# Optimization experiments

Measured on AMD Instinct MI355X. Metric: run time of the kernel, lower is better.

## Reference

```python
import jax, jax.numpy as jnp
import numpy as np

K = 1048576          # number of shooting particles (k); x also has K points
LR = 0.25            # fixed-point gradient-descent learning rate
N_ITERS = 20         # nr_of_fixed_point_iterations
nl = jnp.tanh        # nonlinearity='tanh'


def _advect(z, t1, b1, t2, b2):
    # z: [n, 2, 1]; t*: [2,2]; b*: [2,1]. dot z = theta1 @ nl(theta2 @ z + b2) + b1
    return jnp.matmul(t1, nl(jnp.matmul(t2, z) + b2)) + b1


def _lagrangian(t1, b1, t2, b2, q, p, invK, invKb):
    eye = jnp.eye(2, dtype=t1.dtype)
    v1 = t1.reshape(-1)
    v2 = (t2 - eye).reshape(-1)
    kinetic = 0.5 * (v1 @ invK @ v1 + v2 @ invK @ v2
                     + b1[:, 0] @ invKb @ b1[:, 0] + b2[:, 0] @ invKb @ b2[:, 0])
    potential = jnp.mean(p * _advect(q, t1, b1, t2, b2))
    return kinetic - potential


def _run_fixed_point(q, p, t1, b1, t2, b2, invK, invKb):
    grad_fn = jax.grad(_lagrangian, argnums=(0, 1, 2, 3))
    def step(carry, _):
        t1, b1, t2, b2 = carry
        g1, gb1, g2, gb2 = grad_fn(t1, b1, t2, b2, q, p, invK, invKb)
        return (t1 - LR * g1, b1 - LR * gb1, t2 - LR * g2, b2 - LR * gb2), None
    carry, _ = jax.lax.scan(step, (t1, b1, t2, b2), None, length=N_ITERS)
    return carry


def setup_inputs() -> dict:
    key = jax.random.key(0)
    k1, k2, k3, k4, k5 = jax.random.split(key, 5)
    inp = jax.random.normal(k1, (3 * K, 1, 2), dtype=jnp.float32)
    return {
        "t": jnp.zeros((1,), dtype=jnp.float32),
        "inp": inp,
        "theta1_init": jax.random.normal(k2, (2, 2), dtype=jnp.float32),
        "bias1_init": jax.random.normal(k3, (2, 1), dtype=jnp.float32),
        "theta2_init": jax.random.normal(k4, (2, 2), dtype=jnp.float32),
        "bias2_init": jax.random.normal(k5, (2, 1), dtype=jnp.float32),
        "inv_Kbar": jnp.eye(4, dtype=jnp.float32),    # Kbar = I(d^2) -> inverse = I
        "inv_Kbar_b": jnp.eye(2, dtype=jnp.float32),  # Kbar_b = I(d) -> inverse = I
        "k": K,
    }


def reference(t, inp, theta1_init, bias1_init, theta2_init, bias2_init,
              inv_Kbar, inv_Kbar_b, k):
    qt, pt, xt = inp[:k], inp[k:2 * k], inp[2 * k:]
    q = jnp.swapaxes(qt, 1, 2)  # [k, 2, 1]
    p = jnp.swapaxes(pt, 1, 2)
    x = jnp.swapaxes(xt, 1, 2)

    def final_thetas(qv):
        return _run_fixed_point(qv, p, theta1_init, bias1_init,
                                theta2_init, bias2_init, inv_Kbar, inv_Kbar_b)

    t1, b1, t2, b2 = final_thetas(q)

    # dot_p = dL/dq of the final Lagrangian, including dependence of the
    # fixed-point thetas on q (torch uses create_graph=True throughout).
    def L_of_q(qv):
        ft1, fb1, ft2, fb2 = final_thetas(qv)
        return _lagrangian(ft1, fb1, ft2, fb2, qv, p, inv_Kbar, inv_Kbar_b)

    dot_p = jax.grad(L_of_q)(q)
    dot_x = _advect(x, t1, b1, t2, b2)
    dot_q = _advect(q, t1, b1, t2, b2)

    return jnp.concatenate([jnp.swapaxes(dot_q, 1, 2),
                            jnp.swapaxes(dot_p, 1, 2),
                            jnp.swapaxes(dot_x, 1, 2)], axis=0)
```

## Files before the change

kernel.cpp:

```cpp
#include <hip/hip_runtime.h>


#define LR 0.25f
#define NIT 20
#define RTPB 512
#define NBR 256

typedef float v2f __attribute__((ext_vector_type(2)));

__device__ __forceinline__ v2f tanh2(v2f x){
    v2f e;
    e.x = __expf(x.x + x.x);
    e.y = __expf(x.y + x.y);
    v2f d = e + 1.0f;
    v2f r;
    r.x = __builtin_amdgcn_rcpf(d.x);
    r.y = __builtin_amdgcn_rcpf(d.y);
    return 1.0f - (r + r);
}

#define DPP_ADD(x, ctrl) ((x) + __int_as_float(__builtin_amdgcn_update_dpp(0, __float_as_int(x), (ctrl), 0xF, 0xF, true)))
__device__ __forceinline__ float wave_sum64(float x){
    x = DPP_ADD(x, 0x111);
    x = DPP_ADD(x, 0x112);
    x = DPP_ADD(x, 0x114);
    x = DPP_ADD(x, 0x118);
    x = DPP_ADD(x, 0x142);
    x = DPP_ADD(x, 0x143);
    return x;
}

__device__ __forceinline__ void compute_grad(const float* s, const float* th,
                                             const float* ksym, const float* ksymb,
                                             float c, float* g){
    const float Ivec[4]={1.f,0.f,0.f,1.f};
    #pragma unroll
    for(int j=0;j<4;j++){
        float kv=0.f;
        #pragma unroll
        for(int m=0;m<4;m++) kv += ksym[j*4+m]*th[m];
        g[j] = kv - c*s[j];
    }
    #pragma unroll
    for(int i2=0;i2<2;i2++)
        g[4+i2] = ksymb[i2*2+0]*th[4] + ksymb[i2*2+1]*th[5] - c*s[4+i2];
    #pragma unroll
    for(int j=0;j<4;j++){
        float kv=0.f;
        #pragma unroll
        for(int m=0;m<4;m++) kv += ksym[j*4+m]*(th[6+m]-Ivec[m]);
        g[6+j] = kv - c*s[6+j];
    }
    #pragma unroll
    for(int i2=0;i2<2;i2++)
        g[10+i2] = ksymb[i2*2+0]*th[10] + ksymb[i2*2+1]*th[11] - c*s[10+i2];
}

__device__ __forceinline__ void accum_sample2(v2f Q0, v2f Q1, v2f P0, v2f P1,
    float t1_00,float t1_01,float t1_10,float t1_11,
    float t2_00,float t2_01,float t2_10,float t2_11,float b2_0,float b2_1,
    v2f (&acc)[36]){
    v2f u0 = t2_00*Q0 + t2_01*Q1 + b2_0;
    v2f u1 = t2_10*Q0 + t2_11*Q1 + b2_1;
    v2f h0 = tanh2(u0), h1 = tanh2(u1);
    v2f s0 = 1.0f - h0*h0, s1 = 1.0f - h1*h1;
    v2f a0 = t1_00*P0 + t1_10*P1;
    v2f a1 = t1_01*P0 + t1_11*P1;
    v2f w0 = a0*s0, w1 = a1*s1;
    v2f r0 = -2.0f*(a0*h0)*s0, r1 = -2.0f*(a1*h1)*s1;
    acc[0]+=P0*h0; acc[1]+=P0*h1; acc[2]+=P1*h0; acc[3]+=P1*h1;
    acc[4]+=P0;    acc[5]+=P1;
    acc[6]+=w0*Q0; acc[7]+=w0*Q1; acc[8]+=w1*Q0; acc[9]+=w1*Q1;
    acc[10]+=w0;   acc[11]+=w1;
    v2f ps00=P0*s0, ps01=P0*s1, ps10=P1*s0, ps11=P1*s1;
    acc[12]+=ps00*Q0; acc[13]+=ps00*Q1; acc[14]+=ps01*Q0; acc[15]+=ps01*Q1;
    acc[16]+=ps10*Q0; acc[17]+=ps10*Q1; acc[18]+=ps11*Q0; acc[19]+=ps11*Q1;
    acc[20]+=ps00; acc[21]+=ps01; acc[22]+=ps10; acc[23]+=ps11;
    v2f r0q0=r0*Q0, r1q0=r1*Q0;
    acc[24]+=r0q0*Q0; acc[25]+=r0q0*Q1; acc[26]+=r0*(Q1*Q1);
    acc[27]+=r1q0*Q0; acc[28]+=r1q0*Q1; acc[29]+=r1*(Q1*Q1);
    acc[30]+=r0q0; acc[31]+=r0*Q1; acc[32]+=r1q0; acc[33]+=r1*Q1;
    acc[34]+=r0; acc[35]+=r1;
}

__global__ __launch_bounds__(RTPB) void k_reduce(
    const float4* __restrict__ q4, const float4* __restrict__ p4, int nv4,
    const float* __restrict__ t1i, const float* __restrict__ b1i,
    const float* __restrict__ t2i, const float* __restrict__ b2i,
    const float* __restrict__ invK, const float* __restrict__ invKb,
    const float* __restrict__ theta_prev,
    const float* __restrict__ part_prev,
    float* __restrict__ part_out,
    float* __restrict__ theta_out,
    float c)
{
    const int tid = threadIdx.x;
    const int NT = gridDim.x*RTPB;
    const int gtid = blockIdx.x*RTPB + tid;

    __shared__ float ths[12];
    __shared__ float sgv[12];
    __shared__ float tsum[12][33];
    __shared__ float red[RTPB/64][36];
    __shared__ float ks[16], ksb[4];

    if(!part_prev){
        if(tid < 12){
            float v = (tid<4)? t1i[tid] : (tid<6)? b1i[tid-4]
                    : (tid<10)? t2i[tid-6] : b2i[tid-10];
            ths[tid] = v;
            if(blockIdx.x==0) theta_out[tid] = v;
        }
        __syncthreads();
    }else{
        if(tid < 16) ks[tid]  = 0.5f*(invK[tid]  + invK[(tid&3)*4 + (tid>>2)]);
        if(tid < 4)  ksb[tid] = 0.5f*(invKb[tid] + invKb[(tid&1)*2 + (tid>>1)]);
        if(tid < 12*32){
            int j = tid >> 5, ch = tid & 31;
            const float* col = part_prev + j*NBR;
            float s = 0.f;
            #pragma unroll
            for(int i = 0; i < NBR/32; i++) s += col[ch + i*32];
            tsum[j][ch] = s;
        }
        __syncthreads();
        if(tid < 12){
            float s = 0.f;
            #pragma unroll
            for(int ch=0; ch<32; ch++) s += tsum[tid][ch];
            sgv[tid] = s;
        }
        __syncthreads();
        if(tid == 0){
            float g[12], tp[12];
            #pragma unroll
            for(int j=0;j<12;j++) tp[j] = theta_prev[j];
            compute_grad(sgv, tp, ks, ksb, c, g);
            #pragma unroll
            for(int j=0;j<12;j++){
                float t = tp[j] - LR*g[j];
                ths[j] = t;
                if(blockIdx.x==0) theta_out[j] = t;
            }
        }
        __syncthreads();
    }

    const float t1_00=ths[0], t1_01=ths[1], t1_10=ths[2], t1_11=ths[3];
    const float t2_00=ths[6], t2_01=ths[7], t2_10=ths[8], t2_11=ths[9];
    const float b2_0=ths[10], b2_1=ths[11];

    v2f acc[36];
    #pragma unroll
    for(int j=0;j<36;j++) acc[j] = (v2f){0.f, 0.f};

    if(nv4 == 4*NT){
        float4 qd[4], pd[4];
        #pragma unroll
        for(int s=0;s<4;s++){ qd[s]=q4[gtid + s*NT]; pd[s]=p4[gtid + s*NT]; }
        #pragma unroll
        for(int s=0;s<4;s++){
            v2f Q0={qd[s].x,qd[s].z}, Q1={qd[s].y,qd[s].w};
            v2f P0={pd[s].x,pd[s].z}, P1={pd[s].y,pd[s].w};
            accum_sample2(Q0,Q1,P0,P1,
                t1_00,t1_01,t1_10,t1_11,t2_00,t2_01,t2_10,t2_11,b2_0,b2_1,acc);
        }
    }else{
        for(int j = gtid; j < nv4; j += NT){
            float4 qq = q4[j], pp = p4[j];
            v2f Q0={qq.x,qq.z}, Q1={qq.y,qq.w};
            v2f P0={pp.x,pp.z}, P1={pp.y,pp.w};
            accum_sample2(Q0,Q1,P0,P1,
                t1_00,t1_01,t1_10,t1_11,t2_00,t2_01,t2_10,t2_11,b2_0,b2_1,acc);
        }
    }

    const int wave = tid >> 6;
    float wres[36];
    #pragma unroll
    for(int j=0;j<36;j++) wres[j] = wave_sum64(acc[j].x + acc[j].y);
    if((tid & 63) == 63){
        #pragma unroll
        for(int j=0;j<36;j++) red[wave][j] = wres[j];
    }
    __syncthreads();
    if(tid < 36){
        float sum = 0.f;
        #pragma unroll
        for(int w=0; w<RTPB/64; w++) sum += red[w][tid];
        part_out[tid*NBR + blockIdx.x] = sum;
    }
}

__global__ __launch_bounds__(1024) void k_backfold(
    const float* __restrict__ part,
    const float* __restrict__ thetaAll,
    const float* __restrict__ invK, const float* __restrict__ invKb,
    float* __restrict__ pk_g, float c)
{
    const int tid = threadIdx.x;
    const int wave = tid >> 6, lane = tid & 63;
    __shared__ float sums[(NIT+1)*36];
    __shared__ float ks[16], ksb[4];
    if(tid < 16) ks[tid]  = 0.5f*(invK[tid]  + invK[(tid&3)*4 + (tid>>2)]);
    if(tid < 4)  ksb[tid] = 0.5f*(invKb[tid] + invKb[(tid&1)*2 + (tid>>1)]);

    for(int seg = wave; seg < (NIT+1)*36; seg += 16){
        const float* base = part + (size_t)seg*NBR;
        float s = 0.f;
        #pragma unroll
        for(int i = 0; i < NBR/64; i++) s += base[lane + i*64];
        s = wave_sum64(s);
        if(lane == 63) sums[seg] = s;
    }
    __syncthreads();

    if(tid == 0){
        float lv[12];
        compute_grad(sums + 20*36, thetaAll + 20*12, ks, ksb, c, lv);
        for(int k=NIT-1;k>=0;k--){
            const float* s = sums + k*36;
            const float* T = thetaAll + k*12;
            float* P = pk_g + k*20;
            P[0]=T[0]; P[1]=T[1]; P[2]=T[2]; P[3]=T[3];
            P[4]=T[6]; P[5]=T[7]; P[6]=T[8]; P[7]=T[9];
            P[8]=T[10]; P[9]=T[11];
            P[10]=lv[0]; P[11]=lv[1]; P[12]=lv[2]; P[13]=lv[3];
            P[14]=lv[6]; P[15]=lv[7]; P[16]=lv[8]; P[17]=lv[9];
            P[18]=lv[10]; P[19]=lv[11];
            float H[12];
            for(int a=0;a<2;a++)for(int b=0;b<2;b++){
                int j=a*2+b;
                float data = s[12+a*4+b*2+0]*lv[6+b*2+0]
                           + s[12+a*4+b*2+1]*lv[6+b*2+1]
                           + s[20+a*2+b]*lv[10+b];
                float kv=0.f;
                for(int m=0;m<4;m++) kv += ks[j*4+m]*lv[m];
                H[j]=kv - c*data;
            }
            H[4] = ksb[0]*lv[4] + ksb[1]*lv[5];
            H[5] = ksb[2]*lv[4] + ksb[3]*lv[5];
            for(int cc=0;cc<2;cc++)for(int d=0;d<2;d++){
                int j=cc*2+d;
                float term1 = lv[0+cc]*s[12+0*4+cc*2+d] + lv[2+cc]*s[12+1*4+cc*2+d];
                float term2 = lv[6+cc*2+0]*s[24+cc*3+(0+d)] + lv[6+cc*2+1]*s[24+cc*3+(1+d)];
                float term3 = lv[10+cc]*s[30+cc*2+d];
                float kv=0.f;
                for(int m=0;m<4;m++) kv += ks[j*4+m]*lv[6+m];
                H[6+j]=kv - c*(term1+term2+term3);
            }
            for(int cc=0;cc<2;cc++){
                float z1 = lv[0+cc]*s[20+0*2+cc] + lv[2+cc]*s[20+1*2+cc];
                float z2 = lv[6+cc*2+0]*s[30+cc*2+0] + lv[6+cc*2+1]*s[30+cc*2+1];
                float z3 = lv[10+cc]*s[34+cc];
                float kv = ksb[cc*2+0]*lv[10] + ksb[cc*2+1]*lv[11];
                H[10+cc]=kv - c*(z1+z2+z3);
            }
            for(int j=0;j<12;j++) lv[j] -= LR*H[j];
        }
    }
}

__device__ __forceinline__ void bk_step2(v2f Q0, v2f Q1, v2f P0, v2f P1,
    float t1_00,float t1_01,float t1_10,float t1_11,
    float t2_00,float t2_01,float t2_10,float t2_11,float b2_0,float b2_1,
    float L1_00,float L1_01,float L1_10,float L1_11,
    float L2_00,float L2_01,float L2_10,float L2_11,float lb2_0,float lb2_1,
    v2f &B0, v2f &B1){
    v2f u0 = t2_00*Q0 + t2_01*Q1 + b2_0;
    v2f u1 = t2_10*Q0 + t2_11*Q1 + b2_1;
    v2f h0 = tanh2(u0), h1 = tanh2(u1);
    v2f s0 = 1.0f - h0*h0, s1 = 1.0f - h1*h1;
    v2f a0 = t1_00*P0 + t1_10*P1;
    v2f a1 = t1_01*P0 + t1_11*P1;
    v2f w0 = a0*s0, w1 = a1*s1;
    v2f r0 = -2.0f*(a0*h0)*s0, r1 = -2.0f*(a1*h1)*s1;
    v2f lp0 = L1_00*P0 + L1_10*P1;
    v2f lp1 = L1_01*P0 + L1_11*P1;
    v2f z0 = L2_00*Q0 + L2_01*Q1 + lb2_0;
    v2f z1 = L2_10*Q0 + L2_11*Q1 + lb2_1;
    v2f m0 = lp0*s0 + r0*z0;
    v2f m1 = lp1*s1 + r1*z1;
    B0 += t2_00*m0 + t2_10*m1 + L2_00*w0 + L2_10*w1;
    B1 += t2_01*m0 + t2_11*m1 + L2_01*w0 + L2_11*w1;
}

__global__ __launch_bounds__(256) void k_final(
    const float4* __restrict__ q4, const float4* __restrict__ p4,
    const float4* __restrict__ x4, int nv4,
    const float4* __restrict__ pk4,
    const float4* __restrict__ th20_4,
    float4* __restrict__ oq, float4* __restrict__ op, float4* __restrict__ ox,
    float c)
{
    __shared__ float4 pkS[NIT*5];
    __shared__ float4 t20[3];
    for(int j=threadIdx.x;j<NIT*5;j+=blockDim.x) pkS[j]=pk4[j];
    if(threadIdx.x<3) t20[threadIdx.x]=th20_4[threadIdx.x];
    __syncthreads();

    const int NT = gridDim.x*blockDim.x;
    const int j1 = blockIdx.x*blockDim.x + threadIdx.x;
    const int j2 = j1 + NT;
    const bool v1 = (j1 < nv4), v2 = (j2 < nv4);

    v2f Q0a,Q1a,P0a,P1a, Q0b,Q1b,P0b,P1b;
    if(v1){ float4 qq=q4[j1], pp=p4[j1];
        Q0a=(v2f){qq.x,qq.z}; Q1a=(v2f){qq.y,qq.w};
        P0a=(v2f){pp.x,pp.z}; P1a=(v2f){pp.y,pp.w}; }
    if(v2){ float4 qq=q4[j2], pp=p4[j2];
        Q0b=(v2f){qq.x,qq.z}; Q1b=(v2f){qq.y,qq.w};
        P0b=(v2f){pp.x,pp.z}; P1b=(v2f){pp.y,pp.w}; }

    v2f B0a={0.f,0.f},B1a={0.f,0.f},B0b={0.f,0.f},B1b={0.f,0.f};
    #pragma unroll 4
    for(int k=0;k<NIT;k++){
        float4 P0=pkS[k*5+0], P1=pkS[k*5+1], P2=pkS[k*5+2], P3=pkS[k*5+3], P4v=pkS[k*5+4];
        float t1_00=P0.x,t1_01=P0.y,t1_10=P0.z,t1_11=P0.w;
        float t2_00=P1.x,t2_01=P1.y,t2_10=P1.z,t2_11=P1.w;
        float b2_0=P2.x,b2_1=P2.y;
        float L1_00=P2.z,L1_01=P2.w,L1_10=P3.x,L1_11=P3.y;
        float L2_00=P3.z,L2_01=P3.w,L2_10=P4v.x,L2_11=P4v.y,lb2_0=P4v.z,lb2_1=P4v.w;
        if(v1) bk_step2(Q0a,Q1a,P0a,P1a,
                t1_00,t1_01,t1_10,t1_11,t2_00,t2_01,t2_10,t2_11,b2_0,b2_1,
                L1_00,L1_01,L1_10,L1_11,L2_00,L2_01,L2_10,L2_11,lb2_0,lb2_1,B0a,B1a);
        if(v2) bk_step2(Q0b,Q1b,P0b,P1b,
                t1_00,t1_01,t1_10,t1_11,t2_00,t2_01,t2_10,t2_11,b2_0,b2_1,
                L1_00,L1_01,L1_10,L1_11,L2_00,L2_01,L2_10,L2_11,lb2_0,lb2_1,B0b,B1b);
    }

    float4 Ta=t20[0], Tb=t20[1], Tc=t20[2];
    float t1_00=Ta.x,t1_01=Ta.y,t1_10=Ta.z,t1_11=Ta.w,b1_0=Tb.x,b1_1=Tb.y;
    float t2_00=Tb.z,t2_01=Tb.w,t2_10=Tc.x,t2_11=Tc.y,b2_0=Tc.z,b2_1=Tc.w;

    #pragma unroll
    for(int sl=0; sl<2; sl++){
        bool v = sl? v2 : v1;
        if(!v) continue;
        int j = sl? j2 : j1;
        v2f Q0 = sl? Q0b:Q0a, Q1 = sl? Q1b:Q1a, P0 = sl? P0b:P0a, P1 = sl? P1b:P1a;
        v2f Bs0 = sl? B0b:B0a, Bs1 = sl? B1b:B1a;
        v2f u0 = t2_00*Q0 + t2_01*Q1 + b2_0;
        v2f u1 = t2_10*Q0 + t2_11*Q1 + b2_1;
        v2f h0 = tanh2(u0), h1 = tanh2(u1);
        v2f s0 = 1.0f - h0*h0, s1 = 1.0f - h1*h1;
        v2f a0 = t1_00*P0 + t1_10*P1;
        v2f a1 = t1_01*P0 + t1_11*P1;
        v2f w0 = a0*s0, w1 = a1*s1;
        v2f dq0 = t1_00*h0 + t1_01*h1 + b1_0;
        v2f dq1 = t1_10*h0 + t1_11*h1 + b1_1;
        v2f dp0 = c*(LR*Bs0 - (t2_00*w0 + t2_10*w1));
        v2f dp1 = c*(LR*Bs1 - (t2_01*w0 + t2_11*w1));
        oq[j] = make_float4(dq0.x, dq1.x, dq0.y, dq1.y);
        op[j] = make_float4(dp0.x, dp1.x, dp0.y, dp1.y);
        float4 xx = x4[j];
        v2f X0={xx.x,xx.z}, X1={xx.y,xx.w};
        v2f xu0 = t2_00*X0 + t2_01*X1 + b2_0;
        v2f xu1 = t2_10*X0 + t2_11*X1 + b2_1;
        v2f xh0 = tanh2(xu0), xh1 = tanh2(xu1);
        v2f xd0 = t1_00*xh0 + t1_01*xh1 + b1_0;
        v2f xd1 = t1_10*xh0 + t1_11*xh1 + b1_1;
        ox[j] = make_float4(xd0.x, xd1.x, xd0.y, xd1.y);
    }
}

extern "C" void kernel_launch(void* const* d_in, const int* in_sizes, int n_in,
                              void* d_out, int out_size, void* d_ws, size_t ws_size,
                              hipStream_t stream) {
    const float* inp = (const float*)d_in[1];
    const int K = in_sizes[1]/6;
    const int nv4 = K >> 1;

    const float4* q4 = (const float4*)inp;
    const float4* p4 = (const float4*)(inp + 2*(size_t)K);
    const float4* x4 = (const float4*)(inp + 4*(size_t)K);

    float* part  = (float*)d_ws;
    float* theta = part + (size_t)(NIT+1)*36*NBR;
    float* pk    = theta + 252;
    const float c = 1.0f/(2.0f*(float)K);

    const float* t1i = (const float*)d_in[2];
    const float* b1i = (const float*)d_in[3];
    const float* t2i = (const float*)d_in[4];
    const float* b2i = (const float*)d_in[5];
    const float* invK = (const float*)d_in[6];
    const float* invKb= (const float*)d_in[7];

    for(int k=0;k<=NIT;k++){
        const float* th_prev = (k==0) ? nullptr : theta + (k-1)*12;
        const float* pt_prev = (k==0) ? nullptr : part + (size_t)(k-1)*36*NBR;
        k_reduce<<<NBR,RTPB,0,stream>>>(q4, p4, nv4,
                                        t1i, b1i, t2i, b2i, invK, invKb,
                                        th_prev, pt_prev,
                                        part + (size_t)k*36*NBR, theta + k*12, c);
    }
    k_backfold<<<1,1024,0,stream>>>(part, theta, invK, invKb, pk, c);

    float* out = (float*)d_out;
    int fthreads = (nv4 + 1)/2;
    int fblk = (fthreads + 255)/256;
    k_final<<<fblk,256,0,stream>>>(q4, p4, x4, nv4,
                                   (const float4*)pk, (const float4*)(theta + NIT*12),
                                   (float4*)out, (float4*)(out + 2*(size_t)K),
                                   (float4*)(out + 4*(size_t)K), c);
}
```

Before: 281.9 us.

## Skip unused second-order sums at ends, issue loads early, XCD-aware block mapping

Templates the reduction kernel so the first and last fixed-point passes accumulate only the 12 first-order sums, because the backward fold never reads their 24 second-order terms. The backfold skips summing those unused partials and exits before computing the k=0 Hessian term. Input loads are hoisted above the theta-update prologue so memory latency overlaps the gradient computation. Both the reduce and final kernels remap block indices so that blocks sharing an XCD (blockIdx & 7) cover a contiguous slice, aiming for better L2 locality on the MI355X.

```diff
diff --git a/kernel.cpp b/kernel.cpp
--- a/kernel.cpp
+++ b/kernel.cpp
@@ -56,10 +56,11 @@
         g[10+i2] = ksymb[i2*2+0]*th[10] + ksymb[i2*2+1]*th[11] - c*s[10+i2];
 }
 
+template<bool FULL>
 __device__ __forceinline__ void accum_sample2(v2f Q0, v2f Q1, v2f P0, v2f P1,
     float t1_00,float t1_01,float t1_10,float t1_11,
     float t2_00,float t2_01,float t2_10,float t2_11,float b2_0,float b2_1,
-    v2f (&acc)[36]){
+    v2f* acc){
     v2f u0 = t2_00*Q0 + t2_01*Q1 + b2_0;
     v2f u1 = t2_10*Q0 + t2_11*Q1 + b2_1;
     v2f h0 = tanh2(u0), h1 = tanh2(u1);
@@ -67,22 +68,25 @@
     v2f a0 = t1_00*P0 + t1_10*P1;
     v2f a1 = t1_01*P0 + t1_11*P1;
     v2f w0 = a0*s0, w1 = a1*s1;
-    v2f r0 = -2.0f*(a0*h0)*s0, r1 = -2.0f*(a1*h1)*s1;
     acc[0]+=P0*h0; acc[1]+=P0*h1; acc[2]+=P1*h0; acc[3]+=P1*h1;
     acc[4]+=P0;    acc[5]+=P1;
     acc[6]+=w0*Q0; acc[7]+=w0*Q1; acc[8]+=w1*Q0; acc[9]+=w1*Q1;
     acc[10]+=w0;   acc[11]+=w1;
-    v2f ps00=P0*s0, ps01=P0*s1, ps10=P1*s0, ps11=P1*s1;
-    acc[12]+=ps00*Q0; acc[13]+=ps00*Q1; acc[14]+=ps01*Q0; acc[15]+=ps01*Q1;
-    acc[16]+=ps10*Q0; acc[17]+=ps10*Q1; acc[18]+=ps11*Q0; acc[19]+=ps11*Q1;
-    acc[20]+=ps00; acc[21]+=ps01; acc[22]+=ps10; acc[23]+=ps11;
-    v2f r0q0=r0*Q0, r1q0=r1*Q0;
-    acc[24]+=r0q0*Q0; acc[25]+=r0q0*Q1; acc[26]+=r0*(Q1*Q1);
-    acc[27]+=r1q0*Q0; acc[28]+=r1q0*Q1; acc[29]+=r1*(Q1*Q1);
-    acc[30]+=r0q0; acc[31]+=r0*Q1; acc[32]+=r1q0; acc[33]+=r1*Q1;
-    acc[34]+=r0; acc[35]+=r1;
-}
-
+    if(FULL){
+        v2f r0 = -2.0f*(a0*h0)*s0, r1 = -2.0f*(a1*h1)*s1;
+        v2f ps00=P0*s0, ps01=P0*s1, ps10=P1*s0, ps11=P1*s1;
+        acc[12]+=ps00*Q0; acc[13]+=ps00*Q1; acc[14]+=ps01*Q0; acc[15]+=ps01*Q1;
+        acc[16]+=ps10*Q0; acc[17]+=ps10*Q1; acc[18]+=ps11*Q0; acc[19]+=ps11*Q1;
+        acc[20]+=ps00; acc[21]+=ps01; acc[22]+=ps10; acc[23]+=ps11;
+        v2f r0q0=r0*Q0, r1q0=r1*Q0;
+        acc[24]+=r0q0*Q0; acc[25]+=r0q0*Q1; acc[26]+=r0*(Q1*Q1);
+        acc[27]+=r1q0*Q0; acc[28]+=r1q0*Q1; acc[29]+=r1*(Q1*Q1);
+        acc[30]+=r0q0; acc[31]+=r0*Q1; acc[32]+=r1q0; acc[33]+=r1*Q1;
+        acc[34]+=r0; acc[35]+=r1;
+    }
+}
+
+template<bool FULL>
 __global__ __launch_bounds__(RTPB) void k_reduce(
     const float4* __restrict__ q4, const float4* __restrict__ p4, int nv4,
     const float* __restrict__ t1i, const float* __restrict__ b1i,
@@ -94,15 +98,25 @@
     float* __restrict__ theta_out,
     float c)
 {
+    constexpr int NS = FULL ? 36 : 12;
     const int tid = threadIdx.x;
     const int NT = gridDim.x*RTPB;
-    const int gtid = blockIdx.x*RTPB + tid;
 
     __shared__ float ths[12];
     __shared__ float sgv[12];
     __shared__ float tsum[12][33];
-    __shared__ float red[RTPB/64][36];
+    __shared__ float red[RTPB/64][NS];
     __shared__ float ks[16], ksb[4];
+
+    const bool structured = (nv4 == NBR*RTPB*4);
+    float4 qd[4], pd[4];
+    if(structured){
+        const int xcd = blockIdx.x & 7, bi = blockIdx.x >> 3;
+        const int sliceSz = nv4 >> 3;
+        const int base = xcd*sliceSz + bi*RTPB + tid;
+        #pragma unroll
+        for(int s=0;s<4;s++){ qd[s]=q4[base + s*(32*RTPB)]; pd[s]=p4[base + s*(32*RTPB)]; }
+    }
 
     if(!part_prev){
         if(tid < 12){
@@ -150,41 +164,38 @@
     const float t2_00=ths[6], t2_01=ths[7], t2_10=ths[8], t2_11=ths[9];
     const float b2_0=ths[10], b2_1=ths[11];
 
-    v2f acc[36];
-    #pragma unroll
-    for(int j=0;j<36;j++) acc[j] = (v2f){0.f, 0.f};
-
-    if(nv4 == 4*NT){
-        float4 qd[4], pd[4];
-        #pragma unroll
-        for(int s=0;s<4;s++){ qd[s]=q4[gtid + s*NT]; pd[s]=p4[gtid + s*NT]; }
+    v2f acc[NS];
+    #pragma unroll
+    for(int j=0;j<NS;j++) acc[j] = (v2f){0.f, 0.f};
+
+    if(structured){
         #pragma unroll
         for(int s=0;s<4;s++){
             v2f Q0={qd[s].x,qd[s].z}, Q1={qd[s].y,qd[s].w};
             v2f P0={pd[s].x,pd[s].z}, P1={pd[s].y,pd[s].w};
-            accum_sample2(Q0,Q1,P0,P1,
+            accum_sample2<FULL>(Q0,Q1,P0,P1,
                 t1_00,t1_01,t1_10,t1_11,t2_00,t2_01,t2_10,t2_11,b2_0,b2_1,acc);
         }
     }else{
-        for(int j = gtid; j < nv4; j += NT){
+        for(int j = blockIdx.x*RTPB + tid; j < nv4; j += NT){
             float4 qq = q4[j], pp = p4[j];
             v2f Q0={qq.x,qq.z}, Q1={qq.y,qq.w};
             v2f P0={pp.x,pp.z}, P1={pp.y,pp.w};
-            accum_sample2(Q0,Q1,P0,P1,
+            accum_sample2<FULL>(Q0,Q1,P0,P1,
                 t1_00,t1_01,t1_10,t1_11,t2_00,t2_01,t2_10,t2_11,b2_0,b2_1,acc);
         }
     }
 
     const int wave = tid >> 6;
-    float wres[36];
-    #pragma unroll
-    for(int j=0;j<36;j++) wres[j] = wave_sum64(acc[j].x + acc[j].y);
+    float wres[NS];
+    #pragma unroll
+    for(int j=0;j<NS;j++) wres[j] = wave_sum64(acc[j].x + acc[j].y);
     if((tid & 63) == 63){
         #pragma unroll
-        for(int j=0;j<36;j++) red[wave][j] = wres[j];
+        for(int j=0;j<NS;j++) red[wave][j] = wres[j];
     }
     __syncthreads();
-    if(tid < 36){
+    if(tid < NS){
         float sum = 0.f;
         #pragma unroll
         for(int w=0; w<RTPB/64; w++) sum += red[w][tid];
@@ -206,11 +217,14 @@
     if(tid < 4)  ksb[tid] = 0.5f*(invKb[tid] + invKb[(tid&1)*2 + (tid>>1)]);
 
     for(int seg = wave; seg < (NIT+1)*36; seg += 16){
-        const float* base = part + (size_t)seg*NBR;
+        int row = seg/36, col = seg - row*36;
         float s = 0.f;
-        #pragma unroll
-        for(int i = 0; i < NBR/64; i++) s += base[lane + i*64];
-        s = wave_sum64(s);
+        if(col < 12 || (row >= 1 && row <= 19)){
+            const float* base = part + (size_t)seg*NBR;
+            #pragma unroll
+            for(int i = 0; i < NBR/64; i++) s += base[lane + i*64];
+            s = wave_sum64(s);
+        }
         if(lane == 63) sums[seg] = s;
     }
     __syncthreads();
@@ -228,6 +242,7 @@
             P[10]=lv[0]; P[11]=lv[1]; P[12]=lv[2]; P[13]=lv[3];
             P[14]=lv[6]; P[15]=lv[7]; P[16]=lv[8]; P[17]=lv[9];
             P[18]=lv[10]; P[19]=lv[11];
+            if(k==0) break;
             float H[12];
             for(int a=0;a<2;a++)for(int b=0;b<2;b++){
                 int j=a*2+b;
@@ -288,8 +303,7 @@
 __global__ __launch_bounds__(256) void k_final(
     const float4* __restrict__ q4, const float4* __restrict__ p4,
     const float4* __restrict__ x4, int nv4,
-    const float4* __restrict__ pk4,
-    const float4* __restrict__ th20_4,
+    const float4* __restrict__ pk4, const float4* __restrict__ th20_4,
     float4* __restrict__ oq, float4* __restrict__ op, float4* __restrict__ ox,
     float c)
 {
@@ -299,9 +313,16 @@
     if(threadIdx.x<3) t20[threadIdx.x]=th20_4[threadIdx.x];
     __syncthreads();
 
-    const int NT = gridDim.x*blockDim.x;
-    const int j1 = blockIdx.x*blockDim.x + threadIdx.x;
-    const int j2 = j1 + NT;
+    int j1, j2;
+    const int fblk = gridDim.x;
+    if((nv4 & 511) == 0 && (fblk & 7) == 0 && nv4 == fblk*512){
+        const int xcd = blockIdx.x & 7, bi = blockIdx.x >> 3;
+        j1 = xcd*(nv4>>3) + bi*512 + threadIdx.x;
+        j2 = j1 + 256;
+    }else{
+        j1 = blockIdx.x*blockDim.x + threadIdx.x;
+        j2 = j1 + fblk*256;
+    }
     const bool v1 = (j1 < nv4), v2 = (j2 < nv4);
 
     v2f Q0a,Q1a,P0a,P1a, Q0b,Q1b,P0b,P1b;
@@ -390,10 +411,14 @@
     for(int k=0;k<=NIT;k++){
         const float* th_prev = (k==0) ? nullptr : theta + (k-1)*12;
         const float* pt_prev = (k==0) ? nullptr : part + (size_t)(k-1)*36*NBR;
-        k_reduce<<<NBR,RTPB,0,stream>>>(q4, p4, nv4,
-                                        t1i, b1i, t2i, b2i, invK, invKb,
-                                        th_prev, pt_prev,
-                                        part + (size_t)k*36*NBR, theta + k*12, c);
+        float* po = part + (size_t)k*36*NBR;
+        float* to = theta + k*12;
+        if(k==0 || k==NIT)
+            k_reduce<false><<<NBR,RTPB,0,stream>>>(q4, p4, nv4,
+                t1i, b1i, t2i, b2i, invK, invKb, th_prev, pt_prev, po, to, c);
+        else
+            k_reduce<true><<<NBR,RTPB,0,stream>>>(q4, p4, nv4,
+                t1i, b1i, t2i, b2i, invK, invKb, th_prev, pt_prev, po, to, c);
     }
     k_backfold<<<1,1024,0,stream>>>(part, theta, invK, invKb, pk, c);
 
```

Result: no change. 284.1 us (+0.8%).

## Fuse all iterations, backfold and final pass into one persistent kernel

Applied to the files above, without the earlier changes.

Replaces the 21 reduction launches, the backfold kernel and the final kernel with one persistent 256-block kernel. A two-level atomic grid barrier separates iterations. Each thread loads its q/p samples into registers once and reuses them across all fixed-point iterations and the backward pass, which removes repeated global reads and per-launch overhead. The cost is that the kernel relies on all 256 blocks being co-resident (launch_bounds with 2 blocks per CU), and every iteration now waits on a spin barrier.

```diff
diff --git a/kernel.cpp b/kernel.cpp
--- a/kernel.cpp
+++ b/kernel.cpp
@@ -3,8 +3,11 @@
 
 #define LR 0.25f
 #define NIT 20
-#define RTPB 512
-#define NBR 256
+#define TPB 512
+#define NBLK 256
+#define NTH (NBLK*TPB)
+#define NBR NBLK
+#define SL 4
 
 typedef float v2f __attribute__((ext_vector_type(2)));
 
@@ -30,6 +33,37 @@
     return x;
 }
 
+__device__ __forceinline__ float ld_agent(const float* p){
+    return __hip_atomic_load(p, __ATOMIC_RELAXED, __HIP_MEMORY_SCOPE_AGENT);
+}
+
+__device__ __forceinline__ void grid_barrier(unsigned* bar, unsigned epoch, int grp){
+    __syncthreads();
+    if(threadIdx.x==0){
+        unsigned prev = __hip_atomic_fetch_add(&bar[grp*32], 1u,
+                            __ATOMIC_ACQ_REL, __HIP_MEMORY_SCOPE_AGENT);
+        if(prev == epoch*(NBLK/8) - 1u){
+            unsigned p2 = __hip_atomic_fetch_add(&bar[16*32], 1u,
+                              __ATOMIC_ACQ_REL, __HIP_MEMORY_SCOPE_AGENT);
+            if(p2 == epoch*8u - 1u){
+                __hip_atomic_store(&bar[17*32], epoch,
+                                   __ATOMIC_RELEASE, __HIP_MEMORY_SCOPE_AGENT);
+            }else{
+                while(__hip_atomic_load(&bar[17*32], __ATOMIC_ACQUIRE,
+                                        __HIP_MEMORY_SCOPE_AGENT) < epoch)
+                    __builtin_amdgcn_s_sleep(8);
+            }
+            __hip_atomic_store(&bar[(8+grp)*32], epoch,
+                               __ATOMIC_RELEASE, __HIP_MEMORY_SCOPE_AGENT);
+        }else{
+            while(__hip_atomic_load(&bar[(8+grp)*32], __ATOMIC_ACQUIRE,
+                                    __HIP_MEMORY_SCOPE_AGENT) < epoch)
+                __builtin_amdgcn_s_sleep(8);
+        }
+    }
+    __syncthreads();
+}
+
 __device__ __forceinline__ void compute_grad(const float* s, const float* th,
                                              const float* ksym, const float* ksymb,
                                              float c, float* g){
@@ -59,7 +93,7 @@
 __device__ __forceinline__ void accum_sample2(v2f Q0, v2f Q1, v2f P0, v2f P1,
     float t1_00,float t1_01,float t1_10,float t1_11,
     float t2_00,float t2_01,float t2_10,float t2_11,float b2_0,float b2_1,
-    v2f (&acc)[36]){
+    v2f* acc){
     v2f u0 = t2_00*Q0 + t2_01*Q1 + b2_0;
     v2f u1 = t2_10*Q0 + t2_11*Q1 + b2_1;
     v2f h0 = tanh2(u0), h1 = tanh2(u1);
@@ -81,184 +115,6 @@
     acc[27]+=r1q0*Q0; acc[28]+=r1q0*Q1; acc[29]+=r1*(Q1*Q1);
     acc[30]+=r0q0; acc[31]+=r0*Q1; acc[32]+=r1q0; acc[33]+=r1*Q1;
     acc[34]+=r0; acc[35]+=r1;
-}
-
-__global__ __launch_bounds__(RTPB) void k_reduce(
-    const float4* __restrict__ q4, const float4* __restrict__ p4, int nv4,
-    const float* __restrict__ t1i, const float* __restrict__ b1i,
-    const float* __restrict__ t2i, const float* __restrict__ b2i,
-    const float* __restrict__ invK, const float* __restrict__ invKb,
-    const float* __restrict__ theta_prev,
-    const float* __restrict__ part_prev,
-    float* __restrict__ part_out,
-    float* __restrict__ theta_out,
-    float c)
-{
-    const int tid = threadIdx.x;
-    const int NT = gridDim.x*RTPB;
-    const int gtid = blockIdx.x*RTPB + tid;
-
-    __shared__ float ths[12];
-    __shared__ float sgv[12];
-    __shared__ float tsum[12][33];
-    __shared__ float red[RTPB/64][36];
-    __shared__ float ks[16], ksb[4];
-
-    if(!part_prev){
-        if(tid < 12){
-            float v = (tid<4)? t1i[tid] : (tid<6)? b1i[tid-4]
-                    : (tid<10)? t2i[tid-6] : b2i[tid-10];
-            ths[tid] = v;
-            if(blockIdx.x==0) theta_out[tid] = v;
-        }
-        __syncthreads();
-    }else{
-        if(tid < 16) ks[tid]  = 0.5f*(invK[tid]  + invK[(tid&3)*4 + (tid>>2)]);
-        if(tid < 4)  ksb[tid] = 0.5f*(invKb[tid] + invKb[(tid&1)*2 + (tid>>1)]);
-        if(tid < 12*32){
-            int j = tid >> 5, ch = tid & 31;
-            const float* col = part_prev + j*NBR;
-            float s = 0.f;
-            #pragma unroll
-            for(int i = 0; i < NBR/32; i++) s += col[ch + i*32];
-            tsum[j][ch] = s;
-        }
-        __syncthreads();
-        if(tid < 12){
-            float s = 0.f;
-            #pragma unroll
-            for(int ch=0; ch<32; ch++) s += tsum[tid][ch];
-            sgv[tid] = s;
-        }
-        __syncthreads();
-        if(tid == 0){
-            float g[12], tp[12];
-            #pragma unroll
-            for(int j=0;j<12;j++) tp[j] = theta_prev[j];
-            compute_grad(sgv, tp, ks, ksb, c, g);
-            #pragma unroll
-            for(int j=0;j<12;j++){
-                float t = tp[j] - LR*g[j];
-                ths[j] = t;
-                if(blockIdx.x==0) theta_out[j] = t;
-            }
-        }
-        __syncthreads();
-    }
-
-    const float t1_00=ths[0], t1_01=ths[1], t1_10=ths[2], t1_11=ths[3];
-    const float t2_00=ths[6], t2_01=ths[7], t2_10=ths[8], t2_11=ths[9];
-    const float b2_0=ths[10], b2_1=ths[11];
-
-    v2f acc[36];
-    #pragma unroll
-    for(int j=0;j<36;j++) acc[j] = (v2f){0.f, 0.f};
-
-    if(nv4 == 4*NT){
-        float4 qd[4], pd[4];
-        #pragma unroll
-        for(int s=0;s<4;s++){ qd[s]=q4[gtid + s*NT]; pd[s]=p4[gtid + s*NT]; }
-        #pragma unroll
-        for(int s=0;s<4;s++){
-            v2f Q0={qd[s].x,qd[s].z}, Q1={qd[s].y,qd[s].w};
-            v2f P0={pd[s].x,pd[s].z}, P1={pd[s].y,pd[s].w};
-            accum_sample2(Q0,Q1,P0,P1,
-                t1_00,t1_01,t1_10,t1_11,t2_00,t2_01,t2_10,t2_11,b2_0,b2_1,acc);
-        }
-    }else{
-        for(int j = gtid; j < nv4; j += NT){
-            float4 qq = q4[j], pp = p4[j];
-            v2f Q0={qq.x,qq.z}, Q1={qq.y,qq.w};
-            v2f P0={pp.x,pp.z}, P1={pp.y,pp.w};
-            accum_sample2(Q0,Q1,P0,P1,
-                t1_00,t1_01,t1_10,t1_11,t2_00,t2_01,t2_10,t2_11,b2_0,b2_1,acc);
-        }
-    }
-
-    const int wave = tid >> 6;
-    float wres[36];
-    #pragma unroll
-    for(int j=0;j<36;j++) wres[j] = wave_sum64(acc[j].x + acc[j].y);
-    if((tid & 63) == 63){
-        #pragma unroll
-        for(int j=0;j<36;j++) red[wave][j] = wres[j];
-    }
-    __syncthreads();
-    if(tid < 36){
-        float sum = 0.f;
-        #pragma unroll
-        for(int w=0; w<RTPB/64; w++) sum += red[w][tid];
-        part_out[tid*NBR + blockIdx.x] = sum;
-    }
-}
-
-__global__ __launch_bounds__(1024) void k_backfold(
-    const float* __restrict__ part,
-    const float* __restrict__ thetaAll,
-    const float* __restrict__ invK, const float* __restrict__ invKb,
-    float* __restrict__ pk_g, float c)
-{
-    const int tid = threadIdx.x;
-    const int wave = tid >> 6, lane = tid & 63;
-    __shared__ float sums[(NIT+1)*36];
-    __shared__ float ks[16], ksb[4];
-    if(tid < 16) ks[tid]  = 0.5f*(invK[tid]  + invK[(tid&3)*4 + (tid>>2)]);
-    if(tid < 4)  ksb[tid] = 0.5f*(invKb[tid] + invKb[(tid&1)*2 + (tid>>1)]);
-
-    for(int seg = wave; seg < (NIT+1)*36; seg += 16){
-        const float* base = part + (size_t)seg*NBR;
-        float s = 0.f;
-        #pragma unroll
-        for(int i = 0; i < NBR/64; i++) s += base[lane + i*64];
-        s = wave_sum64(s);
-        if(lane == 63) sums[seg] = s;
-    }
-    __syncthreads();
-
-    if(tid == 0){
-        float lv[12];
-        compute_grad(sums + 20*36, thetaAll + 20*12, ks, ksb, c, lv);
-        for(int k=NIT-1;k>=0;k--){
-            const float* s = sums + k*36;
-            const float* T = thetaAll + k*12;
-            float* P = pk_g + k*20;
-            P[0]=T[0]; P[1]=T[1]; P[2]=T[2]; P[3]=T[3];
-            P[4]=T[6]; P[5]=T[7]; P[6]=T[8]; P[7]=T[9];
-            P[8]=T[10]; P[9]=T[11];
-            P[10]=lv[0]; P[11]=lv[1]; P[12]=lv[2]; P[13]=lv[3];
-            P[14]=lv[6]; P[15]=lv[7]; P[16]=lv[8]; P[17]=lv[9];
-            P[18]=lv[10]; P[19]=lv[11];
-            float H[12];
-            for(int a=0;a<2;a++)for(int b=0;b<2;b++){
-                int j=a*2+b;
-                float data = s[12+a*4+b*2+0]*lv[6+b*2+0]
-                           + s[12+a*4+b*2+1]*lv[6+b*2+1]
-                           + s[20+a*2+b]*lv[10+b];
-                float kv=0.f;
-                for(int m=0;m<4;m++) kv += ks[j*4+m]*lv[m];
-                H[j]=kv - c*data;
-            }
-            H[4] = ksb[0]*lv[4] + ksb[1]*lv[5];
-            H[5] = ksb[2]*lv[4] + ksb[3]*lv[5];
-            for(int cc=0;cc<2;cc++)for(int d=0;d<2;d++){
-                int j=cc*2+d;
-                float term1 = lv[0+cc]*s[12+0*4+cc*2+d] + lv[2+cc]*s[12+1*4+cc*2+d];
-                float term2 = lv[6+cc*2+0]*s[24+cc*3+(0+d)] + lv[6+cc*2+1]*s[24+cc*3+(1+d)];
-                float term3 = lv[10+cc]*s[30+cc*2+d];
-                float kv=0.f;
-                for(int m=0;m<4;m++) kv += ks[j*4+m]*lv[6+m];
-                H[6+j]=kv - c*(term1+term2+term3);
-            }
-            for(int cc=0;cc<2;cc++){
-                float z1 = lv[0+cc]*s[20+0*2+cc] + lv[2+cc]*s[20+1*2+cc];
-                float z2 = lv[6+cc*2+0]*s[30+cc*2+0] + lv[6+cc*2+1]*s[30+cc*2+1];
-                float z3 = lv[10+cc]*s[34+cc];
-                float kv = ksb[cc*2+0]*lv[10] + ksb[cc*2+1]*lv[11];
-                H[10+cc]=kv - c*(z1+z2+z3);
-            }
-            for(int j=0;j<12;j++) lv[j] -= LR*H[j];
-        }
-    }
 }
 
 __device__ __forceinline__ void bk_step2(v2f Q0, v2f Q1, v2f P0, v2f P1,
@@ -285,82 +141,282 @@
     B1 += t2_01*m0 + t2_11*m1 + L2_01*w0 + L2_11*w1;
 }
 
-__global__ __launch_bounds__(256) void k_final(
+__global__ __launch_bounds__(TPB, 2) void k_fused(
     const float4* __restrict__ q4, const float4* __restrict__ p4,
     const float4* __restrict__ x4, int nv4,
-    const float4* __restrict__ pk4,
-    const float4* __restrict__ th20_4,
+    const float* __restrict__ t1i, const float* __restrict__ b1i,
+    const float* __restrict__ t2i, const float* __restrict__ b2i,
+    const float* __restrict__ invK, const float* __restrict__ invKb,
+    float* __restrict__ part, float* __restrict__ theta_g,
+    float* __restrict__ pk_g, unsigned* __restrict__ bar,
     float4* __restrict__ oq, float4* __restrict__ op, float4* __restrict__ ox,
     float c)
 {
-    __shared__ float4 pkS[NIT*5];
-    __shared__ float4 t20[3];
-    for(int j=threadIdx.x;j<NIT*5;j+=blockDim.x) pkS[j]=pk4[j];
-    if(threadIdx.x<3) t20[threadIdx.x]=th20_4[threadIdx.x];
+    const int tid = threadIdx.x, bid = blockIdx.x;
+    const int grp = bid & 7;
+    const int lane = tid & 63, wave = tid >> 6;
+    const int gtid = bid*TPB + tid;
+
+    __shared__ float ths[12], sgv[12], tsum[12][33];
+    __shared__ float red[TPB/64][36];
+    __shared__ float ks[16], ksb[4];
+    __shared__ float sums[(NIT+1)*36];
+    __shared__ __align__(16) float pkS[NIT*20];
+
+    float4 qd[SL], pd[SL];
+    bool val[SL];
+    #pragma unroll
+    for(int s=0;s<SL;s++){
+        int j = gtid + s*NTH;
+        val[s] = (j < nv4);
+        int jc = val[s] ? j : 0;
+        qd[s]=q4[jc]; pd[s]=p4[jc];
+        if(!val[s]){ pd[s].x=0.f; pd[s].y=0.f; pd[s].z=0.f; pd[s].w=0.f; }
+    }
+
+    if(tid<16) ks[tid]  = 0.5f*(invK[tid]  + invK[(tid&3)*4 + (tid>>2)]);
+    if(tid<4)  ksb[tid] = 0.5f*(invKb[tid] + invKb[(tid&1)*2 + (tid>>1)]);
+
+    for(int k=0;k<=NIT;k++){
+        if(k==0){
+            if(tid<12){
+                float v = (tid<4)? t1i[tid] : (tid<6)? b1i[tid-4]
+                        : (tid<10)? t2i[tid-6] : b2i[tid-10];
+                ths[tid] = v;
+                if(bid==0) theta_g[tid] = v;
+            }
+        }else{
+            if(tid < 384){
+                int j = tid >> 5, ch = tid & 31;
+                const float* col = part + (size_t)((k-1)*36 + j)*NBR;
+                float s = 0.f;
+                #pragma unroll
+                for(int i=0;i<NBR/32;i++) s += ld_agent(&col[ch + i*32]);
+                tsum[j][ch] = s;
+            }
+            __syncthreads();
+            if(tid < 12){
+                float s = 0.f;
+                #pragma unroll
+                for(int ch=0; ch<32; ch++) s += tsum[tid][ch];
+                sgv[tid] = s;
+            }
+            __syncthreads();
+            if(tid == 0){
+                float g[12], tp[12];
+                #pragma unroll
+                for(int j=0;j<12;j++) tp[j] = ths[j];
+                compute_grad(sgv, tp, ks, ksb, c, g);
+                #pragma unroll
+                for(int j=0;j<12;j++){
+                    float t = tp[j] - LR*g[j];
+                    ths[j] = t;
+                    if(bid==0) theta_g[k*12+j] = t;
+                }
+            }
+        }
+        __syncthreads();
+
+        const float t1_00=ths[0], t1_01=ths[1], t1_10=ths[2], t1_11=ths[3];
+        const float t2_00=ths[6], t2_01=ths[7], t2_10=ths[8], t2_11=ths[9];
+        const float b2_0=ths[10], b2_1=ths[11];
+
+        v2f acc[36];
+        #pragma unroll
+        for(int j=0;j<36;j++) acc[j] = (v2f){0.f,0.f};
+        #pragma unroll
+        for(int s=0;s<SL;s++){
+            v2f Q0={qd[s].x,qd[s].z}, Q1={qd[s].y,qd[s].w};
+            v2f P0={pd[s].x,pd[s].z}, P1={pd[s].y,pd[s].w};
+            accum_sample2(Q0,Q1,P0,P1,
+                t1_00,t1_01,t1_10,t1_11,t2_00,t2_01,t2_10,t2_11,b2_0,b2_1,acc);
+        }
+        for(int j = SL*NTH + gtid; j < nv4; j += NTH){
+            float4 qq=q4[j], pp=p4[j];
+            v2f Q0={qq.x,qq.z}, Q1={qq.y,qq.w};
+            v2f P0={pp.x,pp.z}, P1={pp.y,pp.w};
+            accum_sample2(Q0,Q1,P0,P1,
+                t1_00,t1_01,t1_10,t1_11,t2_00,t2_01,t2_10,t2_11,b2_0,b2_1,acc);
+        }
+
+        float wres[36];
+        #pragma unroll
+        for(int j=0;j<36;j++) wres[j] = wave_sum64(acc[j].x + acc[j].y);
+        if(lane == 63){
+            #pragma unroll
+            for(int j=0;j<36;j++) red[wave][j] = wres[j];
+        }
+        __syncthreads();
+        if(tid < 36){
+            float sum = 0.f;
+            #pragma unroll
+            for(int w=0; w<TPB/64; w++) sum += red[w][tid];
+            part[((size_t)k*36 + tid)*NBR + bid] = sum;
+        }
+        grid_barrier(bar, (unsigned)(k+1), grp);
+    }
+
+    if(bid == 0){
+        for(int seg = wave; seg < (NIT+1)*36; seg += TPB/64){
+            const float* base = part + (size_t)seg*NBR;
+            float s = 0.f;
+            #pragma unroll
+            for(int i=0;i<NBR/64;i++) s += ld_agent(&base[lane + i*64]);
+            s = wave_sum64(s);
+            if(lane==63) sums[seg] = s;
+        }
+        __syncthreads();
+        if(tid == 0){
+            float lv[12];
+            compute_grad(sums + 20*36, theta_g + 20*12, ks, ksb, c, lv);
+            for(int k=NIT-1;k>=0;k--){
+                const float* s = sums + k*36;
+                const float* T = theta_g + k*12;
+                float* P = pk_g + k*20;
+                P[0]=T[0]; P[1]=T[1]; P[2]=T[2]; P[3]=T[3];
+                P[4]=T[6]; P[5]=T[7]; P[6]=T[8]; P[7]=T[9];
+                P[8]=T[10]; P[9]=T[11];
+                P[10]=lv[0]; P[11]=lv[1]; P[12]=lv[2]; P[13]=lv[3];
+                P[14]=lv[6]; P[15]=lv[7]; P[16]=lv[8]; P[17]=lv[9];
+                P[18]=lv[10]; P[19]=lv[11];
+                if(k==0) break;
+                float H[12];
+                for(int a=0;a<2;a++)for(int b=0;b<2;b++){
+                    int j=a*2+b;
+                    float data = s[12+a*4+b*2+0]*lv[6+b*2+0]
+                               + s[12+a*4+b*2+1]*lv[6+b*2+1]
+                               + s[20+a*2+b]*lv[10+b];
+                    float kv=0.f;
+                    for(int m=0;m<4;m++) kv += ks[j*4+m]*lv[m];
+                    H[j]=kv - c*data;
+                }
+                H[4] = ksb[0]*lv[4] + ksb[1]*lv[5];
+                H[5] = ksb[2]*lv[4] + ksb[3]*lv[5];
+                for(int cc=0;cc<2;cc++)for(int d=0;d<2;d++){
+                    int j=cc*2+d;
+                    float term1 = lv[0+cc]*s[12+0*4+cc*2+d] + lv[2+cc]*s[12+1*4+cc*2+d];
+                    float term2 = lv[6+cc*2+0]*s[24+cc*3+(0+d)] + lv[6+cc*2+1]*s[24+cc*3+(1+d)];
+                    float term3 = lv[10+cc]*s[30+cc*2+d];
+                    float kv=0.f;
+                    for(int m=0;m<4;m++) kv += ks[j*4+m]*lv[6+m];
+                    H[6+j]=kv - c*(term1+term2+term3);
+                }
+                for(int cc=0;cc<2;cc++){
+                    float z1 = lv[0+cc]*s[20+0*2+cc] + lv[2+cc]*s[20+1*2+cc];
+                    float z2 = lv[6+cc*2+0]*s[30+cc*2+0] + lv[6+cc*2+1]*s[30+cc*2+1];
+                    float z3 = lv[10+cc]*s[34+cc];
+                    float kv = ksb[cc*2+0]*lv[10] + ksb[cc*2+1]*lv[11];
+                    H[10+cc]=kv - c*(z1+z2+z3);
+                }
+                for(int j=0;j<12;j++) lv[j] -= LR*H[j];
+            }
+        }
+    }
+    grid_barrier(bar, (unsigned)(NIT+2), grp);
+
+    for(int j=tid; j<NIT*20; j+=TPB) pkS[j] = ld_agent(&pk_g[j]);
     __syncthreads();
 
-    const int NT = gridDim.x*blockDim.x;
-    const int j1 = blockIdx.x*blockDim.x + threadIdx.x;
-    const int j2 = j1 + NT;
-    const bool v1 = (j1 < nv4), v2 = (j2 < nv4);
-
-    v2f Q0a,Q1a,P0a,P1a, Q0b,Q1b,P0b,P1b;
-    if(v1){ float4 qq=q4[j1], pp=p4[j1];
-        Q0a=(v2f){qq.x,qq.z}; Q1a=(v2f){qq.y,qq.w};
-        P0a=(v2f){pp.x,pp.z}; P1a=(v2f){pp.y,pp.w}; }
-    if(v2){ float4 qq=q4[j2], pp=p4[j2];
-        Q0b=(v2f){qq.x,qq.z}; Q1b=(v2f){qq.y,qq.w};
-        P0b=(v2f){pp.x,pp.z}; P1b=(v2f){pp.y,pp.w}; }
-
-    v2f B0a={0.f,0.f},B1a={0.f,0.f},B0b={0.f,0.f},B1b={0.f,0.f};
+    float4 xd[SL];
+    #pragma unroll
+    for(int s=0;s<SL;s++){
+        int j = gtid + s*NTH;
+        xd[s] = x4[val[s] ? j : 0];
+    }
+
+    v2f B0[SL], B1[SL];
+    #pragma unroll
+    for(int s=0;s<SL;s++){ B0[s]=(v2f){0.f,0.f}; B1[s]=(v2f){0.f,0.f}; }
+
     #pragma unroll 4
     for(int k=0;k<NIT;k++){
-        float4 P0=pkS[k*5+0], P1=pkS[k*5+1], P2=pkS[k*5+2], P3=pkS[k*5+3], P4v=pkS[k*5+4];
-        float t1_00=P0.x,t1_01=P0.y,t1_10=P0.z,t1_11=P0.w;
-        float t2_00=P1.x,t2_01=P1.y,t2_10=P1.z,t2_11=P1.w;
-        float b2_0=P2.x,b2_1=P2.y;
-        float L1_00=P2.z,L1_01=P2.w,L1_10=P3.x,L1_11=P3.y;
-        float L2_00=P3.z,L2_01=P3.w,L2_10=P4v.x,L2_11=P4v.y,lb2_0=P4v.z,lb2_1=P4v.w;
-        if(v1) bk_step2(Q0a,Q1a,P0a,P1a,
+        const float4* P4 = (const float4*)(pkS + k*20);
+        float4 Pa=P4[0], Pb=P4[1], Pc=P4[2], Pd=P4[3], Pe=P4[4];
+        float t1_00=Pa.x,t1_01=Pa.y,t1_10=Pa.z,t1_11=Pa.w;
+        float t2_00=Pb.x,t2_01=Pb.y,t2_10=Pb.z,t2_11=Pb.w;
+        float b2_0=Pc.x,b2_1=Pc.y;
+        float L1_00=Pc.z,L1_01=Pc.w,L1_10=Pd.x,L1_11=Pd.y;
+        float L2_00=Pd.z,L2_01=Pd.w,L2_10=Pe.x,L2_11=Pe.y,lb2_0=Pe.z,lb2_1=Pe.w;
+        #pragma unroll
+        for(int s=0;s<SL;s++){
+            v2f Q0={qd[s].x,qd[s].z}, Q1={qd[s].y,qd[s].w};
+            v2f P0={pd[s].x,pd[s].z}, P1={pd[s].y,pd[s].w};
+            bk_step2(Q0,Q1,P0,P1,
                 t1_00,t1_01,t1_10,t1_11,t2_00,t2_01,t2_10,t2_11,b2_0,b2_1,
-                L1_00,L1_01,L1_10,L1_11,L2_00,L2_01,L2_10,L2_11,lb2_0,lb2_1,B0a,B1a);
-        if(v2) bk_step2(Q0b,Q1b,P0b,P1b,
-                t1_00,t1_01,t1_10,t1_11,t2_00,t2_01,t2_10,t2_11,b2_0,b2_1,
-                L1_00,L1_01,L1_10,L1_11,L2_00,L2_01,L2_10,L2_11,lb2_0,lb2_1,B0b,B1b);
-    }
-
-    float4 Ta=t20[0], Tb=t20[1], Tc=t20[2];
-    float t1_00=Ta.x,t1_01=Ta.y,t1_10=Ta.z,t1_11=Ta.w,b1_0=Tb.x,b1_1=Tb.y;
-    float t2_00=Tb.z,t2_01=Tb.w,t2_10=Tc.x,t2_11=Tc.y,b2_0=Tc.z,b2_1=Tc.w;
-
-    #pragma unroll
-    for(int sl=0; sl<2; sl++){
-        bool v = sl? v2 : v1;
-        if(!v) continue;
-        int j = sl? j2 : j1;
-        v2f Q0 = sl? Q0b:Q0a, Q1 = sl? Q1b:Q1a, P0 = sl? P0b:P0a, P1 = sl? P1b:P1a;
-        v2f Bs0 = sl? B0b:B0a, Bs1 = sl? B1b:B1a;
+                L1_00,L1_01,L1_10,L1_11,L2_00,L2_01,L2_10,L2_11,lb2_0,lb2_1,
+                B0[s],B1[s]);
+        }
+    }
+
+    {
+        const float t1_00=ths[0],t1_01=ths[1],t1_10=ths[2],t1_11=ths[3];
+        const float b1_0=ths[4],b1_1=ths[5];
+        const float t2_00=ths[6],t2_01=ths[7],t2_10=ths[8],t2_11=ths[9];
+        const float b2_0=ths[10],b2_1=ths[11];
+        #pragma unroll
+        for(int s=0;s<SL;s++){
+            if(!val[s]) continue;
+            int j = gtid + s*NTH;
+            v2f Q0={qd[s].x,qd[s].z}, Q1={qd[s].y,qd[s].w};
+            v2f P0={pd[s].x,pd[s].z}, P1={pd[s].y,pd[s].w};
+            v2f u0 = t2_00*Q0 + t2_01*Q1 + b2_0;
+            v2f u1 = t2_10*Q0 + t2_11*Q1 + b2_1;
+            v2f h0 = tanh2(u0), h1 = tanh2(u1);
+            v2f s0 = 1.0f-h0*h0, s1 = 1.0f-h1*h1;
+            v2f a0 = t1_00*P0 + t1_10*P1;
+            v2f a1 = t1_01*P0 + t1_11*P1;
+            v2f w0 = a0*s0, w1 = a1*s1;
+            v2f dq0 = t1_00*h0 + t1_01*h1 + b1_0;
+            v2f dq1 = t1_10*h0 + t1_11*h1 + b1_1;
+            v2f dp0 = c*(LR*B0[s] - (t2_00*w0 + t2_10*w1));
+            v2f dp1 = c*(LR*B1[s] - (t2_01*w0 + t2_11*w1));
+            oq[j] = make_float4(dq0.x, dq1.x, dq0.y, dq1.y);
+            op[j] = make_float4(dp0.x, dp1.x, dp0.y, dp1.y);
+            v2f X0={xd[s].x,xd[s].z}, X1={xd[s].y,xd[s].w};
+            v2f xu0 = t2_00*X0 + t2_01*X1 + b2_0;
+            v2f xu1 = t2_10*X0 + t2_11*X1 + b2_1;
+            v2f xh0 = tanh2(xu0), xh1 = tanh2(xu1);
+            v2f xd0 = t1_00*xh0 + t1_01*xh1 + b1_0;
+            v2f xd1 = t1_10*xh0 + t1_11*xh1 + b1_1;
+            ox[j] = make_float4(xd0.x, xd1.x, xd0.y, xd1.y);
+        }
+    }
+
+    for(int j = SL*NTH + gtid; j < nv4; j += NTH){
+        float4 qq=q4[j], pp=p4[j], xx=x4[j];
+        v2f Q0={qq.x,qq.z}, Q1={qq.y,qq.w};
+        v2f P0={pp.x,pp.z}, P1={pp.y,pp.w};
+        v2f Bt0={0.f,0.f}, Bt1={0.f,0.f};
+        for(int k=0;k<NIT;k++){
+            const float* P = pkS + k*20;
+            bk_step2(Q0,Q1,P0,P1, P[0],P[1],P[2],P[3], P[4],P[5],P[6],P[7],P[8],P[9],
+                     P[10],P[11],P[12],P[13], P[14],P[15],P[16],P[17],P[18],P[19],
+                     Bt0,Bt1);
+        }
+        const float t1_00=ths[0],t1_01=ths[1],t1_10=ths[2],t1_11=ths[3];
+        const float b1_0=ths[4],b1_1=ths[5];
+        const float t2_00=ths[6],t2_01=ths[7],t2_10=ths[8],t2_11=ths[9];
+        const float b2_0=ths[10],b2_1=ths[11];
         v2f u0 = t2_00*Q0 + t2_01*Q1 + b2_0;
         v2f u1 = t2_10*Q0 + t2_11*Q1 + b2_1;
         v2f h0 = tanh2(u0), h1 = tanh2(u1);
-        v2f s0 = 1.0f - h0*h0, s1 = 1.0f - h1*h1;
+        v2f s0 = 1.0f-h0*h0, s1 = 1.0f-h1*h1;
         v2f a0 = t1_00*P0 + t1_10*P1;
         v2f a1 = t1_01*P0 + t1_11*P1;
         v2f w0 = a0*s0, w1 = a1*s1;
         v2f dq0 = t1_00*h0 + t1_01*h1 + b1_0;
         v2f dq1 = t1_10*h0 + t1_11*h1 + b1_1;
-        v2f dp0 = c*(LR*Bs0 - (t2_00*w0 + t2_10*w1));
-        v2f dp1 = c*(LR*Bs1 - (t2_01*w0 + t2_11*w1));
+        v2f dp0 = c*(LR*Bt0 - (t2_00*w0 + t2_10*w1));
+        v2f dp1 = c*(LR*Bt1 - (t2_01*w0 + t2_11*w1));
         oq[j] = make_float4(dq0.x, dq1.x, dq0.y, dq1.y);
         op[j] = make_float4(dp0.x, dp1.x, dp0.y, dp1.y);
-        float4 xx = x4[j];
         v2f X0={xx.x,xx.z}, X1={xx.y,xx.w};
         v2f xu0 = t2_00*X0 + t2_01*X1 + b2_0;
         v2f xu1 = t2_10*X0 + t2_11*X1 + b2_1;
         v2f xh0 = tanh2(xu0), xh1 = tanh2(xu1);
-        v2f xd0 = t1_00*xh0 + t1_01*xh1 + b1_0;
-        v2f xd1 = t1_10*xh0 + t1_11*xh1 + b1_1;
-        ox[j] = make_float4(xd0.x, xd1.x, xd0.y, xd1.y);
+        v2f o0 = t1_00*xh0 + t1_01*xh1 + b1_0;
+        v2f o1 = t1_10*xh0 + t1_11*xh1 + b1_1;
+        ox[j] = make_float4(o0.x, o1.x, o0.y, o1.y);
     }
 }
 
@@ -378,30 +434,19 @@
     float* part  = (float*)d_ws;
     float* theta = part + (size_t)(NIT+1)*36*NBR;
     float* pk    = theta + 252;
+    size_t barOff = (size_t)(NIT+1)*36*NBR + 252 + 400;
+    barOff = (barOff + 31) & ~(size_t)31;
+    unsigned* bar = (unsigned*)((float*)d_ws + barOff);
     const float c = 1.0f/(2.0f*(float)K);
 
-    const float* t1i = (const float*)d_in[2];
-    const float* b1i = (const float*)d_in[3];
-    const float* t2i = (const float*)d_in[4];
-    const float* b2i = (const float*)d_in[5];
-    const float* invK = (const float*)d_in[6];
-    const float* invKb= (const float*)d_in[7];
-
-    for(int k=0;k<=NIT;k++){
-        const float* th_prev = (k==0) ? nullptr : theta + (k-1)*12;
-        const float* pt_prev = (k==0) ? nullptr : part + (size_t)(k-1)*36*NBR;
-        k_reduce<<<NBR,RTPB,0,stream>>>(q4, p4, nv4,
-                                        t1i, b1i, t2i, b2i, invK, invKb,
-                                        th_prev, pt_prev,
-                                        part + (size_t)k*36*NBR, theta + k*12, c);
-    }
-    k_backfold<<<1,1024,0,stream>>>(part, theta, invK, invKb, pk, c);
+    hipMemsetAsync(bar, 0, 18*32*sizeof(unsigned), stream);
 
     float* out = (float*)d_out;
-    int fthreads = (nv4 + 1)/2;
-    int fblk = (fthreads + 255)/256;
-    k_final<<<fblk,256,0,stream>>>(q4, p4, x4, nv4,
-                                   (const float4*)pk, (const float4*)(theta + NIT*12),
-                                   (float4*)out, (float4*)(out + 2*(size_t)K),
-                                   (float4*)(out + 4*(size_t)K), c);
-}
+    k_fused<<<NBLK, TPB, 0, stream>>>(q4, p4, x4, nv4,
+        (const float*)d_in[2], (const float*)d_in[3],
+        (const float*)d_in[4], (const float*)d_in[5],
+        (const float*)d_in[6], (const float*)d_in[7],
+        part, theta, pk, bar,
+        (float4*)out, (float4*)(out + 2*(size_t)K), (float4*)(out + 4*(size_t)K),
+        c);
+}
```

After: 927.2 us. +228.9%, slower.
